# Kernel tuning notes

Hardware: AMD Instinct MI355X
Metric: run time of the kernel (lower is better)

The kernel has to match this reference:

```python
import jax, jax.numpy as jnp
import numpy as np

B, L, H = 4, 512, 768          # batch, seq_len, bert hidden
S, R = 100, 100                # num candidate spans, num relation pairs
E = 128                        # size embedding dim
TE, TR = 8, 6                  # entity / relation types
MAX_ENT_LEN = 100
NEG = -1e20


def _span_masks(rng, b, n, seq_len, max_len):
    # contiguous span masks with lengths in [1, max_len-1] so sum(-1) < max_len
    starts = rng.integers(0, seq_len - 1, size=(b, n))
    lengths = rng.integers(1, max_len, size=(b, n))
    ends = np.minimum(starts + lengths, seq_len)
    pos = np.arange(seq_len)
    m = (pos[None, None, :] >= starts[..., None]) & (pos[None, None, :] < ends[..., None])
    return jnp.asarray(m.astype(np.int32))


def setup_inputs() -> dict:
    rng = np.random.default_rng(0)
    key = jax.random.key(0)
    k = jax.random.split(key, 6)
    return {
        "last_hidden_state": jax.random.normal(k[0], (B, L, H), jnp.float32),
        "entity_mask": _span_masks(rng, B, S, L, MAX_ENT_LEN),
        "relations": jnp.asarray(rng.integers(0, S, size=(B, R, 2)).astype(np.int32)),
        "relation_context_mask": _span_masks(rng, B, R, L, MAX_ENT_LEN),
        "relation_sample_mask": jnp.asarray(rng.integers(0, 2, size=(B, R)).astype(np.int32)),
        "size_emb": jax.random.normal(k[1], (MAX_ENT_LEN, E), jnp.float32) * 0.02,
        "span_w": jax.random.normal(k[2], (E + 2 * H, TE), jnp.float32) * 0.02,
        "span_b": jnp.zeros((TE,), jnp.float32),
        "rel_w": jax.random.normal(k[3], (2 * E + 3 * H, TR), jnp.float32) * 0.02,
        "rel_b": jnp.zeros((TR,), jnp.float32),
    }


def _masked_max(h, mask):
    # h: [B,L,H], mask: [B,N,L] int {0,1} -> [B,N,H]
    mf = mask[..., None].astype(h.dtype)                       # [B,N,L,1]
    masked = jnp.where(mf == 0, jnp.asarray(NEG, h.dtype), h[:, None] * mf)
    return masked.max(axis=2)


def reference(last_hidden_state, entity_mask, relations, relation_context_mask,
              relation_sample_mask, size_emb, span_w, span_b, rel_w, rel_b):
    b = last_hidden_state.shape[0]
    # ---- entity classification ----
    context = last_hidden_state[:, 0]                          # CLS pooling [B,H]
    entity_size = size_emb[entity_mask.sum(-1)]                # [B,S,E]
    entity = _masked_max(last_hidden_state, entity_mask)       # [B,S,H]
    ctx = jnp.broadcast_to(context[:, None], (b, entity.shape[1], context.shape[-1]))
    entity_repr = jnp.concatenate([entity, ctx, entity_size], axis=-1)
    entity_logit = entity_repr @ span_w + span_b               # [B,S,TE]
    # ---- relation classification ----
    rel_ctx = _masked_max(last_hidden_state, relation_context_mask)  # [B,R,H]
    rel_ctx = jnp.where(relation_sample_mask[..., None] == 1,
                        jnp.zeros((), rel_ctx.dtype), rel_ctx)
    r = relations.shape[1]
    flat = relations.reshape(b, r * 2)                         # [B,2R]
    pair = jnp.take_along_axis(entity, flat[..., None], axis=1).reshape(b, r, -1)      # [B,R,2H]
    pair_size = jnp.take_along_axis(entity_size, flat[..., None], axis=1).reshape(b, r, -1)  # [B,R,2E]
    relation_repr = jnp.concatenate([rel_ctx, pair, pair_size], axis=-1)
    relation_logit = relation_repr @ rel_w + rel_b             # [B,R,TR]
    return entity_logit, relation_logit
```

## Files before the change

kernel.cpp:

```cpp
#include <hip/hip_runtime.h>

#define Bn 4
#define Ln 512
#define Hn 768
#define Sn 100
#define Rn 100
#define En 128
#define TEn 8
#define TRn 6
#define NEGF (-1e20f)
#define W 8
#define NBLK (Ln / W)
#define H4 (Hn / 4)
#define E4 (En / 4)

__device__ __forceinline__ float4 fmax4(float4 a, float4 b) {
    return make_float4(fmaxf(a.x, b.x), fmaxf(a.y, b.y),
                       fmaxf(a.z, b.z), fmaxf(a.w, b.w));
}

__global__ void __launch_bounds__(192)
blockmax_kernel(const float* __restrict__ hid, float* __restrict__ bmax) {
    int bj = blockIdx.x;
    int b = bj / NBLK, j = bj % NBLK;
    int tid = threadIdx.x;
    const float4* src = (const float4*)(hid + ((size_t)b * Ln + j * W) * Hn);
    float4 m = src[tid];
    #pragma unroll
    for (int r = 1; r < W; ++r)
        m = fmax4(m, src[(size_t)r * H4 + tid]);
    ((float4*)(bmax + (size_t)bj * Hn))[tid] = m;
}

__device__ __forceinline__ void scan_span(const int* __restrict__ mask,
                                          int lane, int* start, int* end) {
    const int4* m4 = (const int4*)(mask + lane * 8);
    int4 a = m4[0], c = m4[1];
    int mm[8] = {a.x, a.y, a.z, a.w, c.x, c.y, c.z, c.w};
    int first = 0x7fffffff, last = -1;
    #pragma unroll
    for (int r = 0; r < 8; ++r) {
        if (mm[r] != 0) {
            int row = lane * 8 + r;
            first = min(first, row);
            last = max(last, row);
        }
    }
    #pragma unroll
    for (int off = 1; off < 64; off <<= 1) {
        first = min(first, __shfl_xor(first, off, 64));
        last = max(last, __shfl_xor(last, off, 64));
    }
    *start = first;
    *end = last + 1;
}

__device__ __forceinline__ float4 span_max(const float4* __restrict__ hb4,
                                           const float4* __restrict__ bm4,
                                           int start, int end) {
    float4 m = make_float4(NEGF, NEGF, NEGF, NEGF);
    int jstart = (start + 7) >> 3, jend = end >> 3;
    if (jstart >= jend) {
        for (int r = start; r < end; ++r)
            m = fmax4(m, hb4[(size_t)r * H4]);
        return m;
    }
    int j = jstart;
    for (; j + 2 <= jend; j += 2)
        m = fmax4(m, fmax4(bm4[(size_t)j * H4], bm4[(size_t)(j + 1) * H4]));
    for (; j < jend; ++j)
        m = fmax4(m, bm4[(size_t)j * H4]);
    for (int r = start; r < jstart * W; ++r)
        m = fmax4(m, hb4[(size_t)r * H4]);
    for (int r = jend * W; r < end; ++r)
        m = fmax4(m, hb4[(size_t)r * H4]);
    return m;
}

__global__ void __launch_bounds__(256)
logits_kernel(const float* __restrict__ hid,
              const int* __restrict__ ent_mask,
              const int* __restrict__ rel_mask,
              const int* __restrict__ samp_mask,
              const int* __restrict__ relations,
              const float* __restrict__ size_emb,
              const float* __restrict__ span_w,
              const float* __restrict__ span_b,
              const float* __restrict__ rel_w,
              const float* __restrict__ rel_b,
              const float* __restrict__ bmax,
              float* __restrict__ out_ent,
              float* __restrict__ out_rel) {
    int blk = blockIdx.x;
    int tid = threadIdx.x;
    int lane = tid & 63, wv = tid >> 6;

    __shared__ int se[3][2];
    __shared__ float red[4][TEn];

    if (blk < Bn * Sn) {
        int b = blk / Sn;
        if (wv == 0) {
            int s0, e0;
            scan_span(ent_mask + (size_t)blk * Ln, lane, &s0, &e0);
            if (lane == 0) { se[0][0] = s0; se[0][1] = e0; }
        }
        __syncthreads();
        int start = se[0][0], end = se[0][1];
        int cnt = end - start;

        float acc[TEn];
        #pragma unroll
        for (int t = 0; t < TEn; ++t) acc[t] = 0.0f;

        if (tid < H4) {
            const float4* hb4 = (const float4*)(hid + (size_t)b * Ln * Hn) + tid;
            const float4* bm4 = (const float4*)(bmax + (size_t)b * NBLK * Hn) + tid;
            float4 m = span_max(hb4, bm4, start, end);

            const float* vv = &m.x;
            #pragma unroll
            for (int j = 0; j < 4; ++j) {
                const float4* w4 = (const float4*)(span_w + (size_t)(4 * tid + j) * TEn);
                float4 wa = w4[0], wb = w4[1];
                acc[0] += vv[j] * wa.x; acc[1] += vv[j] * wa.y;
                acc[2] += vv[j] * wa.z; acc[3] += vv[j] * wa.w;
                acc[4] += vv[j] * wb.x; acc[5] += vv[j] * wb.y;
                acc[6] += vv[j] * wb.z; acc[7] += vv[j] * wb.w;
            }
            float4 c = ((const float4*)(hid + (size_t)b * Ln * Hn))[tid];
            const float* cc = &c.x;
            #pragma unroll
            for (int j = 0; j < 4; ++j) {
                const float4* w4 = (const float4*)(span_w + (size_t)(Hn + 4 * tid + j) * TEn);
                float4 wa = w4[0], wb = w4[1];
                acc[0] += cc[j] * wa.x; acc[1] += cc[j] * wa.y;
                acc[2] += cc[j] * wa.z; acc[3] += cc[j] * wa.w;
                acc[4] += cc[j] * wb.x; acc[5] += cc[j] * wb.y;
                acc[6] += cc[j] * wb.z; acc[7] += cc[j] * wb.w;
            }
        } else if (tid >= 192 && tid < 192 + E4) {
            int u = tid - 192;
            float4 sv = ((const float4*)(size_emb + (size_t)cnt * En))[u];
            const float* ss = &sv.x;
            #pragma unroll
            for (int j = 0; j < 4; ++j) {
                const float4* w4 = (const float4*)(span_w + (size_t)(2 * Hn + 4 * u + j) * TEn);
                float4 wa = w4[0], wb = w4[1];
                acc[0] += ss[j] * wa.x; acc[1] += ss[j] * wa.y;
                acc[2] += ss[j] * wa.z; acc[3] += ss[j] * wa.w;
                acc[4] += ss[j] * wb.x; acc[5] += ss[j] * wb.y;
                acc[6] += ss[j] * wb.z; acc[7] += ss[j] * wb.w;
            }
        }

        #pragma unroll
        for (int t = 0; t < TEn; ++t)
            #pragma unroll
            for (int off = 32; off > 0; off >>= 1)
                acc[t] += __shfl_down(acc[t], off, 64);
        if (lane == 0) {
            #pragma unroll
            for (int t = 0; t < TEn; ++t) red[wv][t] = acc[t];
        }
        __syncthreads();
        if (tid < TEn) {
            float s = span_b[tid];
            #pragma unroll
            for (int w = 0; w < 4; ++w) s += red[w][tid];
            out_ent[(size_t)blk * TEn + tid] = s;
        }
    } else {
        int rblk = blk - Bn * Sn;
        int b = rblk / Rn;
        int a0 = relations[rblk * 2 + 0];
        int a1 = relations[rblk * 2 + 1];
        bool samp = (samp_mask[rblk] == 1);

        if (wv == 0) {
            int s0, e0;
            scan_span(ent_mask + ((size_t)b * Sn + a0) * Ln, lane, &s0, &e0);
            if (lane == 0) { se[0][0] = s0; se[0][1] = e0; }
        } else if (wv == 1) {
            int s1, e1;
            scan_span(ent_mask + ((size_t)b * Sn + a1) * Ln, lane, &s1, &e1);
            if (lane == 0) { se[1][0] = s1; se[1][1] = e1; }
        } else if (wv == 2 && !samp) {
            int s2, e2;
            scan_span(rel_mask + (size_t)rblk * Ln, lane, &s2, &e2);
            if (lane == 0) { se[2][0] = s2; se[2][1] = e2; }
        }
        __syncthreads();
        int cnt0 = se[0][1] - se[0][0];
        int cnt1 = se[1][1] - se[1][0];

        float acc[TRn];
        #pragma unroll
        for (int t = 0; t < TRn; ++t) acc[t] = 0.0f;

        if (tid < H4) {
            const float4* hb4 = (const float4*)(hid + (size_t)b * Ln * Hn) + tid;
            const float4* bm4 = (const float4*)(bmax + (size_t)b * NBLK * Hn) + tid;

            float4 ve0 = span_max(hb4, bm4, se[0][0], se[0][1]);
            float4 ve1 = span_max(hb4, bm4, se[1][0], se[1][1]);
            float4 vc = samp ? make_float4(0.f, 0.f, 0.f, 0.f)
                             : span_max(hb4, bm4, se[2][0], se[2][1]);

            const float* vp;
            #pragma unroll
            for (int seg = 0; seg < 3; ++seg) {
                float4 v = (seg == 0) ? vc : (seg == 1) ? ve0 : ve1;
                vp = &v.x;
                int k4 = seg * H4 + tid;
                #pragma unroll
                for (int j = 0; j < 4; ++j) {
                    const float2* wr = (const float2*)(rel_w + (size_t)(4 * k4 + j) * TRn);
                    float2 w0 = wr[0], w1 = wr[1], w2 = wr[2];
                    acc[0] += vp[j] * w0.x; acc[1] += vp[j] * w0.y;
                    acc[2] += vp[j] * w1.x; acc[3] += vp[j] * w1.y;
                    acc[4] += vp[j] * w2.x; acc[5] += vp[j] * w2.y;
                }
            }
        } else if (tid >= 192) {
            int u = tid - 192;
            int k4, srow;
            if (u < E4) { srow = cnt0; k4 = 3 * H4 + u; }
            else        { srow = cnt1; k4 = 3 * H4 + E4 + (u - E4); }
            int uu = (u < E4) ? u : u - E4;
            float4 sv = ((const float4*)(size_emb + (size_t)srow * En))[uu];
            const float* sp = &sv.x;
            #pragma unroll
            for (int j = 0; j < 4; ++j) {
                const float2* wr = (const float2*)(rel_w + (size_t)(4 * k4 + j) * TRn);
                float2 w0 = wr[0], w1 = wr[1], w2 = wr[2];
                acc[0] += sp[j] * w0.x; acc[1] += sp[j] * w0.y;
                acc[2] += sp[j] * w1.x; acc[3] += sp[j] * w1.y;
                acc[4] += sp[j] * w2.x; acc[5] += sp[j] * w2.y;
            }
        }

        #pragma unroll
        for (int t = 0; t < TRn; ++t)
            #pragma unroll
            for (int off = 32; off > 0; off >>= 1)
                acc[t] += __shfl_down(acc[t], off, 64);
        if (lane == 0) {
            #pragma unroll
            for (int t = 0; t < TRn; ++t) red[wv][t] = acc[t];
        }
        __syncthreads();
        if (tid < TRn) {
            float s = rel_b[tid];
            #pragma unroll
            for (int w = 0; w < 4; ++w) s += red[w][tid];
            out_rel[(size_t)rblk * TRn + tid] = s;
        }
    }
}

extern "C" void kernel_launch(void* const* d_in, const int* in_sizes, int n_in,
                              void* d_out, int out_size, void* d_ws, size_t ws_size,
                              hipStream_t stream) {
    const float* hid       = (const float*)d_in[0];
    const int*   ent_mask  = (const int*)d_in[1];
    const int*   relations = (const int*)d_in[2];
    const int*   rel_mask  = (const int*)d_in[3];
    const int*   samp_mask = (const int*)d_in[4];
    const float* size_emb  = (const float*)d_in[5];
    const float* span_w    = (const float*)d_in[6];
    const float* span_b    = (const float*)d_in[7];
    const float* rel_w     = (const float*)d_in[8];
    const float* rel_b     = (const float*)d_in[9];

    float* out = (float*)d_out;
    float* out_ent = out;
    float* out_rel = out + Bn * Sn * TEn;

    float* bmax = (float*)d_ws;

    blockmax_kernel<<<Bn * NBLK, 192, 0, stream>>>(hid, bmax);

    logits_kernel<<<Bn * (Sn + Rn), 256, 0, stream>>>(
        hid, ent_mask, rel_mask, samp_mask, relations, size_emb,
        span_w, span_b, rel_w, rel_b, bmax, out_ent, out_rel);
}
```

Measured before the change: 24.62 us.

## Spread span-max and dot segments across 640 threads with dual accumulators

The logits kernel grows from 256 to 640 threads per block. Each relation block now computes its three span maxima (context, head entity, tail entity) on separate 192-thread groups instead of serially in one group. Entity blocks likewise put the CLS-context dot product on its own thread group. span_max and blockmax now use two independent max accumulators to shorten dependency chains. The trade-off is a ten-wave shared-memory reduction, higher per-block thread count that may cut occupancy, and generic scalar weight loads in place of explicit float4/float2 loads.

```diff
diff --git a/kernel.cpp b/kernel.cpp
--- a/kernel.cpp
+++ b/kernel.cpp
@@ -13,6 +13,7 @@
 #define NBLK (Ln / W)
 #define H4 (Hn / 4)
 #define E4 (En / 4)
+#define NTHR 640
 
 __device__ __forceinline__ float4 fmax4(float4 a, float4 b) {
     return make_float4(fmaxf(a.x, b.x), fmaxf(a.y, b.y),
@@ -25,11 +26,14 @@
     int b = bj / NBLK, j = bj % NBLK;
     int tid = threadIdx.x;
     const float4* src = (const float4*)(hid + ((size_t)b * Ln + j * W) * Hn);
-    float4 m = src[tid];
-    #pragma unroll
-    for (int r = 1; r < W; ++r)
-        m = fmax4(m, src[(size_t)r * H4 + tid]);
-    ((float4*)(bmax + (size_t)bj * Hn))[tid] = m;
+    float4 m0 = src[tid];
+    float4 m1 = src[(size_t)H4 + tid];
+    #pragma unroll
+    for (int r = 2; r < W; r += 2) {
+        m0 = fmax4(m0, src[(size_t)r * H4 + tid]);
+        m1 = fmax4(m1, src[(size_t)(r + 1) * H4 + tid]);
+    }
+    ((float4*)(bmax + (size_t)bj * Hn))[tid] = fmax4(m0, m1);
 }
 
 __device__ __forceinline__ void scan_span(const int* __restrict__ mask,
@@ -58,26 +62,53 @@
 __device__ __forceinline__ float4 span_max(const float4* __restrict__ hb4,
                                            const float4* __restrict__ bm4,
                                            int start, int end) {
-    float4 m = make_float4(NEGF, NEGF, NEGF, NEGF);
+    float4 m0 = make_float4(NEGF, NEGF, NEGF, NEGF);
+    float4 m1 = m0;
     int jstart = (start + 7) >> 3, jend = end >> 3;
     if (jstart >= jend) {
-        for (int r = start; r < end; ++r)
-            m = fmax4(m, hb4[(size_t)r * H4]);
-        return m;
+        int r = start;
+        for (; r + 2 <= end; r += 2) {
+            m0 = fmax4(m0, hb4[(size_t)r * H4]);
+            m1 = fmax4(m1, hb4[(size_t)(r + 1) * H4]);
+        }
+        if (r < end) m0 = fmax4(m0, hb4[(size_t)r * H4]);
+        return fmax4(m0, m1);
     }
     int j = jstart;
-    for (; j + 2 <= jend; j += 2)
-        m = fmax4(m, fmax4(bm4[(size_t)j * H4], bm4[(size_t)(j + 1) * H4]));
-    for (; j < jend; ++j)
-        m = fmax4(m, bm4[(size_t)j * H4]);
-    for (int r = start; r < jstart * W; ++r)
-        m = fmax4(m, hb4[(size_t)r * H4]);
-    for (int r = jend * W; r < end; ++r)
-        m = fmax4(m, hb4[(size_t)r * H4]);
-    return m;
-}
-
-__global__ void __launch_bounds__(256)
+    for (; j + 4 <= jend; j += 4) {
+        m0 = fmax4(m0, fmax4(bm4[(size_t)j * H4], bm4[(size_t)(j + 1) * H4]));
+        m1 = fmax4(m1, fmax4(bm4[(size_t)(j + 2) * H4], bm4[(size_t)(j + 3) * H4]));
+    }
+    for (; j < jend; ++j) m0 = fmax4(m0, bm4[(size_t)j * H4]);
+    int he = jstart * W;
+    int r = start;
+    for (; r + 2 <= he; r += 2) {
+        m0 = fmax4(m0, hb4[(size_t)r * H4]);
+        m1 = fmax4(m1, hb4[(size_t)(r + 1) * H4]);
+    }
+    if (r < he) m0 = fmax4(m0, hb4[(size_t)r * H4]);
+    r = jend * W;
+    for (; r + 2 <= end; r += 2) {
+        m0 = fmax4(m0, hb4[(size_t)r * H4]);
+        m1 = fmax4(m1, hb4[(size_t)(r + 1) * H4]);
+    }
+    if (r < end) m0 = fmax4(m0, hb4[(size_t)r * H4]);
+    return fmax4(m0, m1);
+}
+
+template <int NT>
+__device__ __forceinline__ void dot4(const float4 v, const float* __restrict__ wbase,
+                                     int row, float* acc) {
+    const float* vp = &v.x;
+    #pragma unroll
+    for (int j = 0; j < 4; ++j) {
+        const float* wr = wbase + (size_t)(4 * row + j) * NT;
+        #pragma unroll
+        for (int t = 0; t < NT; ++t) acc[t] += vp[j] * wr[t];
+    }
+}
+
+__global__ void __launch_bounds__(NTHR)
 logits_kernel(const float* __restrict__ hid,
               const int* __restrict__ ent_mask,
               const int* __restrict__ rel_mask,
@@ -96,7 +127,11 @@
     int lane = tid & 63, wv = tid >> 6;
 
     __shared__ int se[3][2];
-    __shared__ float red[4][TEn];
+    __shared__ float red[10][TEn];
+
+    float acc[TEn];
+    #pragma unroll
+    for (int t = 0; t < TEn; ++t) acc[t] = 0.0f;
 
     if (blk < Bn * Sn) {
         int b = blk / Sn;
@@ -109,49 +144,18 @@
         int start = se[0][0], end = se[0][1];
         int cnt = end - start;
 
-        float acc[TEn];
-        #pragma unroll
-        for (int t = 0; t < TEn; ++t) acc[t] = 0.0f;
-
-        if (tid < H4) {
-            const float4* hb4 = (const float4*)(hid + (size_t)b * Ln * Hn) + tid;
+        const float4* hb4 = (const float4*)(hid + (size_t)b * Ln * Hn);
+        if (tid < 192) {
             const float4* bm4 = (const float4*)(bmax + (size_t)b * NBLK * Hn) + tid;
-            float4 m = span_max(hb4, bm4, start, end);
-
-            const float* vv = &m.x;
-            #pragma unroll
-            for (int j = 0; j < 4; ++j) {
-                const float4* w4 = (const float4*)(span_w + (size_t)(4 * tid + j) * TEn);
-                float4 wa = w4[0], wb = w4[1];
-                acc[0] += vv[j] * wa.x; acc[1] += vv[j] * wa.y;
-                acc[2] += vv[j] * wa.z; acc[3] += vv[j] * wa.w;
-                acc[4] += vv[j] * wb.x; acc[5] += vv[j] * wb.y;
-                acc[6] += vv[j] * wb.z; acc[7] += vv[j] * wb.w;
-            }
-            float4 c = ((const float4*)(hid + (size_t)b * Ln * Hn))[tid];
-            const float* cc = &c.x;
-            #pragma unroll
-            for (int j = 0; j < 4; ++j) {
-                const float4* w4 = (const float4*)(span_w + (size_t)(Hn + 4 * tid + j) * TEn);
-                float4 wa = w4[0], wb = w4[1];
-                acc[0] += cc[j] * wa.x; acc[1] += cc[j] * wa.y;
-                acc[2] += cc[j] * wa.z; acc[3] += cc[j] * wa.w;
-                acc[4] += cc[j] * wb.x; acc[5] += cc[j] * wb.y;
-                acc[6] += cc[j] * wb.z; acc[7] += cc[j] * wb.w;
-            }
-        } else if (tid >= 192 && tid < 192 + E4) {
+            float4 m = span_max(hb4 + tid, bm4, start, end);
+            dot4<TEn>(m, span_w, tid, acc);
+        } else if (tid < 384) {
             int u = tid - 192;
+            dot4<TEn>(hb4[u], span_w, H4 + u, acc);
+        } else if (tid < 384 + E4) {
+            int u = tid - 384;
             float4 sv = ((const float4*)(size_emb + (size_t)cnt * En))[u];
-            const float* ss = &sv.x;
-            #pragma unroll
-            for (int j = 0; j < 4; ++j) {
-                const float4* w4 = (const float4*)(span_w + (size_t)(2 * Hn + 4 * u + j) * TEn);
-                float4 wa = w4[0], wb = w4[1];
-                acc[0] += ss[j] * wa.x; acc[1] += ss[j] * wa.y;
-                acc[2] += ss[j] * wa.z; acc[3] += ss[j] * wa.w;
-                acc[4] += ss[j] * wb.x; acc[5] += ss[j] * wb.y;
-                acc[6] += ss[j] * wb.z; acc[7] += ss[j] * wb.w;
-            }
+            dot4<TEn>(sv, span_w, 2 * H4 + u, acc);
         }
 
         #pragma unroll
@@ -167,7 +171,7 @@
         if (tid < TEn) {
             float s = span_b[tid];
             #pragma unroll
-            for (int w = 0; w < 4; ++w) s += red[w][tid];
+            for (int w = 0; w < 10; ++w) s += red[w][tid];
             out_ent[(size_t)blk * TEn + tid] = s;
         }
     } else {
@@ -178,66 +182,47 @@
         bool samp = (samp_mask[rblk] == 1);
 
         if (wv == 0) {
-            int s0, e0;
-            scan_span(ent_mask + ((size_t)b * Sn + a0) * Ln, lane, &s0, &e0);
-            if (lane == 0) { se[0][0] = s0; se[0][1] = e0; }
+            if (!samp) {
+                int s0, e0;
+                scan_span(rel_mask + (size_t)rblk * Ln, lane, &s0, &e0);
+                if (lane == 0) { se[0][0] = s0; se[0][1] = e0; }
+            }
         } else if (wv == 1) {
             int s1, e1;
-            scan_span(ent_mask + ((size_t)b * Sn + a1) * Ln, lane, &s1, &e1);
+            scan_span(ent_mask + ((size_t)b * Sn + a0) * Ln, lane, &s1, &e1);
             if (lane == 0) { se[1][0] = s1; se[1][1] = e1; }
-        } else if (wv == 2 && !samp) {
+        } else if (wv == 2) {
             int s2, e2;
-            scan_span(rel_mask + (size_t)rblk * Ln, lane, &s2, &e2);
+            scan_span(ent_mask + ((size_t)b * Sn + a1) * Ln, lane, &s2, &e2);
             if (lane == 0) { se[2][0] = s2; se[2][1] = e2; }
         }
         __syncthreads();
-        int cnt0 = se[0][1] - se[0][0];
-        int cnt1 = se[1][1] - se[1][0];
-
-        float acc[TRn];
-        #pragma unroll
-        for (int t = 0; t < TRn; ++t) acc[t] = 0.0f;
-
-        if (tid < H4) {
-            const float4* hb4 = (const float4*)(hid + (size_t)b * Ln * Hn) + tid;
-            const float4* bm4 = (const float4*)(bmax + (size_t)b * NBLK * Hn) + tid;
-
-            float4 ve0 = span_max(hb4, bm4, se[0][0], se[0][1]);
-            float4 ve1 = span_max(hb4, bm4, se[1][0], se[1][1]);
-            float4 vc = samp ? make_float4(0.f, 0.f, 0.f, 0.f)
-                             : span_max(hb4, bm4, se[2][0], se[2][1]);
-
-            const float* vp;
-            #pragma unroll
-            for (int seg = 0; seg < 3; ++seg) {
-                float4 v = (seg == 0) ? vc : (seg == 1) ? ve0 : ve1;
-                vp = &v.x;
-                int k4 = seg * H4 + tid;
-                #pragma unroll
-                for (int j = 0; j < 4; ++j) {
-                    const float2* wr = (const float2*)(rel_w + (size_t)(4 * k4 + j) * TRn);
-                    float2 w0 = wr[0], w1 = wr[1], w2 = wr[2];
-                    acc[0] += vp[j] * w0.x; acc[1] += vp[j] * w0.y;
-                    acc[2] += vp[j] * w1.x; acc[3] += vp[j] * w1.y;
-                    acc[4] += vp[j] * w2.x; acc[5] += vp[j] * w2.y;
-                }
+        int cnt0 = se[1][1] - se[1][0];
+        int cnt1 = se[2][1] - se[2][0];
+
+        const float4* hb4 = (const float4*)(hid + (size_t)b * Ln * Hn);
+        const float4* bm4 = (const float4*)(bmax + (size_t)b * NBLK * Hn);
+        if (tid < 192) {
+            if (!samp) {
+                float4 m = span_max(hb4 + tid, bm4 + tid, se[0][0], se[0][1]);
+                dot4<TRn>(m, rel_w, tid, acc);
             }
-        } else if (tid >= 192) {
+        } else if (tid < 384) {
             int u = tid - 192;
-            int k4, srow;
-            if (u < E4) { srow = cnt0; k4 = 3 * H4 + u; }
-            else        { srow = cnt1; k4 = 3 * H4 + E4 + (u - E4); }
-            int uu = (u < E4) ? u : u - E4;
-            float4 sv = ((const float4*)(size_emb + (size_t)srow * En))[uu];
-            const float* sp = &sv.x;
-            #pragma unroll
-            for (int j = 0; j < 4; ++j) {
-                const float2* wr = (const float2*)(rel_w + (size_t)(4 * k4 + j) * TRn);
-                float2 w0 = wr[0], w1 = wr[1], w2 = wr[2];
-                acc[0] += sp[j] * w0.x; acc[1] += sp[j] * w0.y;
-                acc[2] += sp[j] * w1.x; acc[3] += sp[j] * w1.y;
-                acc[4] += sp[j] * w2.x; acc[5] += sp[j] * w2.y;
-            }
+            float4 m = span_max(hb4 + u, bm4 + u, se[1][0], se[1][1]);
+            dot4<TRn>(m, rel_w, H4 + u, acc);
+        } else if (tid < 576) {
+            int u = tid - 384;
+            float4 m = span_max(hb4 + u, bm4 + u, se[2][0], se[2][1]);
+            dot4<TRn>(m, rel_w, 2 * H4 + u, acc);
+        } else if (tid < 576 + E4) {
+            int u = tid - 576;
+            float4 sv = ((const float4*)(size_emb + (size_t)cnt0 * En))[u];
+            dot4<TRn>(sv, rel_w, 3 * H4 + u, acc);
+        } else {
+            int u = tid - 576 - E4;
+            float4 sv = ((const float4*)(size_emb + (size_t)cnt1 * En))[u];
+            dot4<TRn>(sv, rel_w, 3 * H4 + E4 + u, acc);
         }
 
         #pragma unroll
@@ -253,7 +238,7 @@
         if (tid < TRn) {
             float s = rel_b[tid];
             #pragma unroll
-            for (int w = 0; w < 4; ++w) s += red[w][tid];
+            for (int w = 0; w < 10; ++w) s += red[w][tid];
             out_rel[(size_t)rblk * TRn + tid] = s;
         }
     }
@@ -281,7 +266,7 @@
 
     blockmax_kernel<<<Bn * NBLK, 192, 0, stream>>>(hid, bmax);
 
-    logits_kernel<<<Bn * (Sn + Rn), 256, 0, stream>>>(
+    logits_kernel<<<Bn * (Sn + Rn), NTHR, 0, stream>>>(
         hid, ent_mask, rel_mask, samp_mask, relations, size_emb,
         span_w, span_b, rel_w, rel_b, bmax, out_ent, out_rel);
 }
```

Result: faster. 22.25 us (-9.6%).
